# Kernel optimization log

Hardware: AMD Instinct MI355X
Metric: run time of the kernel (lower is better)

The kernel has to match this reference:

```python
import jax, jax.numpy as jnp
import numpy as np

B, D, H, W = 2, 256, 64, 64
NH = 4
EPS = 1e-5


def _ln(x, g, b):
    # LayerNorm over channel dim of NCHW tensor (matches permute->LN(C)->permute)
    mu = jnp.mean(x, axis=1, keepdims=True)
    var = jnp.mean((x - mu) ** 2, axis=1, keepdims=True)
    xn = (x - mu) * jax.lax.rsqrt(var + EPS)
    return xn * g[None, :, None, None] + b[None, :, None, None]


def _conv1x1(x, w, b):
    # w: (out_c, in_c)
    return jnp.einsum('bchw,oc->bohw', x, w) + b[None, :, None, None]


def _dwconv3x3(x, w, b):
    # depthwise 3x3, w: (C, 1, 3, 3)
    y = jax.lax.conv_general_dilated(
        x, w, window_strides=(1, 1), padding='SAME',
        dimension_numbers=('NCHW', 'OIHW', 'NCHW'), feature_group_count=D)
    return y + b[None, :, None, None]


def setup_inputs() -> dict:
    key = jax.random.key(0)
    ks = jax.random.split(key, 12)
    sc = 0.02

    def n(k, shape):
        return jax.random.normal(k, shape, dtype=jnp.float32) * sc

    return {
        'image_embedding': jax.random.normal(ks[0], (B, D, H, W), dtype=jnp.float32),
        'guide': jax.random.normal(ks[1], (B, D, H, W), dtype=jnp.float32),
        'ln1_g': jnp.ones((D,), jnp.float32), 'ln1_b': jnp.zeros((D,), jnp.float32),
        'ln2_g': jnp.ones((D,), jnp.float32), 'ln2_b': jnp.zeros((D,), jnp.float32),
        'qw1': n(ks[2], (D, D)), 'qb1': jnp.zeros((D,), jnp.float32),
        'qw2': n(ks[3], (D, 1, 3, 3)), 'qb2': jnp.zeros((D,), jnp.float32),
        'kw1': n(ks[4], (D, D)), 'kb1': jnp.zeros((D,), jnp.float32),
        'kw2': n(ks[5], (D, 1, 3, 3)), 'kb2': jnp.zeros((D,), jnp.float32),
        'vw1': n(ks[6], (D, D)), 'vb1': jnp.zeros((D,), jnp.float32),
        'vw2': n(ks[7], (D, 1, 3, 3)), 'vb2': jnp.zeros((D,), jnp.float32),
        'ow': n(ks[8], (D, D)), 'ob': jnp.zeros((D,), jnp.float32),
    }


def reference(image_embedding, guide, ln1_g, ln1_b, ln2_g, ln2_b,
              qw1, qb1, qw2, qb2, kw1, kb1, kw2, kb2,
              vw1, vb1, vw2, vb2, ow, ob):
    residual = image_embedding
    x = _ln(image_embedding, ln1_g, ln1_b)
    g = _ln(guide, ln2_g, ln2_b)

    q = _dwconv3x3(_conv1x1(x, qw1, qb1), qw2, qb2)
    k = _dwconv3x3(_conv1x1(g, kw1, kb1), kw2, kb2)
    v = _dwconv3x3(_conv1x1(g, vw1, vb1), vw2, vb2)

    hd = D // NH
    scale = hd ** -0.5

    def to_heads(t):  # (B,C,H,W) -> (B, NH, HW, hd)
        return t.reshape(B, NH, hd, H * W).transpose(0, 1, 3, 2)

    q = to_heads(q) * scale
    k = to_heads(k)
    v = to_heads(v)

    attn = jax.nn.softmax(jnp.einsum('bhnd,bhmd->bhnm', q, k), axis=-1)
    out = jnp.einsum('bhnm,bhmd->bhnd', attn, v)
    out = out.transpose(0, 1, 3, 2).reshape(B, D, H, W)
    out = _conv1x1(out, ow, ob)
    return residual + out
```

## Files before the change

### kernel.cpp

```cpp
#include <hip/hip_runtime.h>
#include <cstdint>
#include <cstddef>

typedef unsigned short u16;
typedef unsigned int u32;
typedef __attribute__((ext_vector_type(8))) short short8;
typedef __attribute__((ext_vector_type(4))) float f32x4;

#define CD 256
#define HWD 4096
#define NHD 4
#define HDD 64

static __device__ __forceinline__ u16 f2b(float f) {
    u32 u = __builtin_bit_cast(u32, f);
    return (u16)((u + 0x7fffu + ((u >> 16) & 1u)) >> 16);
}
static __device__ __forceinline__ float b2f(u16 h) {
    return __builtin_bit_cast(float, (u32)h << 16);
}
static __device__ __forceinline__ u32 pk2(float a, float b) {
    return (u32)f2b(a) | ((u32)f2b(b) << 16);
}
static __device__ __forceinline__ u32 pk2r(float a, float b) {
    u32 ua = __builtin_bit_cast(u32, a) + 0x8000u;
    u32 ub = __builtin_bit_cast(u32, b) + 0x8000u;
    return (ua >> 16) | (ub & 0xffff0000u);
}
static __device__ __forceinline__ float fexp2(float x) {
#if __has_builtin(__builtin_amdgcn_exp2f)
    return __builtin_amdgcn_exp2f(x);
#else
    return __expf(x * 0.69314718056f);
#endif
}
static __device__ __forceinline__ void async16(const void* g, void* l) {
    __builtin_amdgcn_global_load_lds(
        (const __attribute__((address_space(1))) unsigned int*)g,
        (__attribute__((address_space(3))) unsigned int*)l,
        16, 0, 0);
}

__global__ __launch_bounds__(256) void ln_transpose(
    const float* __restrict__ x0, const float* __restrict__ x1,
    const float* __restrict__ g0, const float* __restrict__ b0,
    const float* __restrict__ g1, const float* __restrict__ b1,
    u16* __restrict__ out0, u16* __restrict__ out1)
{
    int bid = blockIdx.x;
    int t = bid >> 7, b = (bid >> 6) & 1, p0 = (bid & 63) << 6;
    const float* x = t ? x1 : x0;
    const float* g = t ? g1 : g0;
    const float* bb = t ? b1 : b0;
    u16* out = t ? out1 : out0;

    int tid = threadIdx.x;
    int tx = tid & 63, ty = tid >> 6;
    const float* xb = x + (size_t)b * CD * HWD + p0 + tx;

    __shared__ float red[2][4][64];
    __shared__ u16 T[256][65];

    float s = 0.f, sq = 0.f;
    #pragma unroll 8
    for (int i = 0; i < 64; ++i) {
        float v = xb[(size_t)(ty * 64 + i) * HWD];
        s += v; sq += v * v;
    }
    red[0][ty][tx] = s; red[1][ty][tx] = sq;
    __syncthreads();
    float st  = red[0][0][tx] + red[0][1][tx] + red[0][2][tx] + red[0][3][tx];
    float sqt = red[1][0][tx] + red[1][1][tx] + red[1][2][tx] + red[1][3][tx];
    float mean = st * (1.f / 256.f);
    float var = sqt * (1.f / 256.f) - mean * mean;
    float rstd = rsqrtf(var + 1e-5f);

    #pragma unroll 8
    for (int i = 0; i < 64; ++i) {
        int c = ty * 64 + i;
        float v = (xb[(size_t)c * HWD] - mean) * rstd * g[c] + bb[c];
        T[c][tx] = f2b(v);
    }
    __syncthreads();

    int pr = tid >> 5, c0 = (tid & 31) * 8;
    #pragma unroll
    for (int pass = 0; pass < 8; ++pass) {
        int p = pass * 8 + pr;
        u16 tmp[8];
        #pragma unroll
        for (int j = 0; j < 8; ++j) tmp[j] = T[c0 + j][p];
        *(uint4*)&out[((size_t)b * HWD + p0 + p) * CD + c0] = *(const uint4*)tmp;
    }
}

__global__ __launch_bounds__(256) void qkv_gemm(
    const u16* __restrict__ xT, const u16* __restrict__ gT,
    const float* __restrict__ qw1, const float* __restrict__ qb1,
    const float* __restrict__ kw1, const float* __restrict__ kb1,
    const float* __restrict__ vw1, const float* __restrict__ vb1,
    u16* __restrict__ q1, u16* __restrict__ k1, u16* __restrict__ v1)
{
    int z = blockIdx.z;
    int mm = z >> 1, b = z & 1;
    const u16* X    = (mm == 0) ? xT : gT;
    const float* W  = (mm == 0) ? qw1 : (mm == 1) ? kw1 : vw1;
    const float* Bi = (mm == 0) ? qb1 : (mm == 1) ? kb1 : vb1;
    u16* Y          = (mm == 0) ? q1 : (mm == 1) ? k1 : v1;

    int n0 = blockIdx.x * 128;
    int p0 = blockIdx.y * 128;

    __shared__ u16 As[128][40];
    __shared__ u16 Bs[128][40];

    int tid = threadIdx.x;
    int lane = tid & 63, w = tid >> 6;
    int wm = w >> 1, wn = w & 1;
    int l15 = lane & 15, quad = lane >> 4;

    f32x4 acc[4][4];
    #pragma unroll
    for (int mi = 0; mi < 4; ++mi)
        #pragma unroll
        for (int nj = 0; nj < 4; ++nj)
            acc[mi][nj] = (f32x4){0.f, 0.f, 0.f, 0.f};

    const u16* Xb = X + (size_t)b * HWD * CD;

    int arow = tid >> 1, akh = (tid & 1) * 16;
    const u16* agp = Xb + (size_t)(p0 + arow) * CD + akh;
    const float* wgp = W + (size_t)(n0 + arow) * CD + akh;

    uint4 ra0 = *(const uint4*)(agp);
    uint4 ra1 = *(const uint4*)(agp + 8);
    float4 rw0 = ((const float4*)wgp)[0], rw1 = ((const float4*)wgp)[1];
    float4 rw2 = ((const float4*)wgp)[2], rw3 = ((const float4*)wgp)[3];

    for (int kt = 0; kt < 8; ++kt) {
        __syncthreads();
        *(uint4*)&As[arow][akh] = ra0;
        *(uint4*)&As[arow][akh + 8] = ra1;
        {
            uint4 qa, qb;
            qa.x = pk2(rw0.x, rw0.y); qa.y = pk2(rw0.z, rw0.w);
            qa.z = pk2(rw1.x, rw1.y); qa.w = pk2(rw1.z, rw1.w);
            qb.x = pk2(rw2.x, rw2.y); qb.y = pk2(rw2.z, rw2.w);
            qb.z = pk2(rw3.x, rw3.y); qb.w = pk2(rw3.z, rw3.w);
            *(uint4*)&Bs[arow][akh] = qa;
            *(uint4*)&Bs[arow][akh + 8] = qb;
        }
        if (kt < 7) {
            const u16* ag2 = agp + (kt + 1) * 32;
            const float* wg2 = wgp + (kt + 1) * 32;
            ra0 = *(const uint4*)(ag2);
            ra1 = *(const uint4*)(ag2 + 8);
            rw0 = ((const float4*)wg2)[0]; rw1 = ((const float4*)wg2)[1];
            rw2 = ((const float4*)wg2)[2]; rw3 = ((const float4*)wg2)[3];
        }
        __syncthreads();

        short8 af[4], bf[4];
        #pragma unroll
        for (int mi = 0; mi < 4; ++mi)
            af[mi] = *(const short8*)&As[wm * 64 + mi * 16 + l15][quad * 8];
        #pragma unroll
        for (int nj = 0; nj < 4; ++nj)
            bf[nj] = *(const short8*)&Bs[wn * 64 + nj * 16 + l15][quad * 8];
        #pragma unroll
        for (int mi = 0; mi < 4; ++mi)
            #pragma unroll
            for (int nj = 0; nj < 4; ++nj)
                acc[mi][nj] = __builtin_amdgcn_mfma_f32_16x16x32_bf16(
                    af[mi], bf[nj], acc[mi][nj], 0, 0, 0);
    }

    u16* Yb = Y + (size_t)b * HWD * CD;
    float bias[4];
    #pragma unroll
    for (int nj = 0; nj < 4; ++nj)
        bias[nj] = Bi[n0 + wn * 64 + nj * 16 + l15];
    #pragma unroll
    for (int mi = 0; mi < 4; ++mi) {
        #pragma unroll
        for (int r = 0; r < 4; ++r) {
            int p = p0 + wm * 64 + mi * 16 + quad * 4 + r;
            #pragma unroll
            for (int nj = 0; nj < 4; ++nj) {
                int ch = n0 + wn * 64 + nj * 16 + l15;
                Yb[(size_t)p * CD + ch] = f2b(acc[mi][nj][r] + bias[nj]);
            }
        }
    }
}

__global__ __launch_bounds__(256) void dwconv_nc(
    const u16* __restrict__ q1, const u16* __restrict__ k1, const u16* __restrict__ v1,
    const float* __restrict__ qw2, const float* __restrict__ qb2,
    const float* __restrict__ kw2, const float* __restrict__ kb2,
    const float* __restrict__ vw2, const float* __restrict__ vb2,
    u16* __restrict__ Q, u16* __restrict__ K, u16* __restrict__ Vt)
{
    int bid = blockIdx.x;
    int which = bid >> 9;
    int b = (bid >> 8) & 1;
    int p0 = (bid & 255) * 16;

    const u16* in = ((which == 0) ? q1 : (which == 1) ? k1 : v1) + (size_t)b * HWD * CD;
    const float* wsrc = (which == 0) ? qw2 : (which == 1) ? kw2 : vw2;
    const float* bsrc = (which == 0) ? qb2 : (which == 1) ? kb2 : vb2;
    float oscale = (which == 0) ? 0.18033688011112042f : 1.0f;

    int c = threadIdx.x;
    float w9[9];
    #pragma unroll
    for (int j = 0; j < 9; ++j) w9[j] = wsrc[c * 9 + j];
    float bias = bsrc[c];

    int h = p0 >> 6, w0 = p0 & 63;

    float accv[16];
    #pragma unroll
    for (int pi = 0; pi < 16; ++pi) accv[pi] = bias;

    #pragma unroll
    for (int dh = -1; dh <= 1; ++dh) {
        int hh = h + dh;
        if (hh < 0 || hh >= 64) continue;
        #pragma unroll
        for (int dw = -1; dw <= 1; ++dw) {
            float wt = w9[(dh + 1) * 3 + (dw + 1)];
            #pragma unroll
            for (int pi = 0; pi < 16; ++pi) {
                int wc = w0 + pi + dw;
                if (wc < 0 || wc >= 64) continue;
                int np = hh * 64 + wc;
                accv[pi] += wt * b2f(in[(size_t)np * CD + c]);
            }
        }
    }

    if (which == 2) {
        u32 w8[8];
        #pragma unroll
        for (int j = 0; j < 8; ++j) w8[j] = pk2(accv[2 * j], accv[2 * j + 1]);
        uint4* dst = (uint4*)(Vt + ((size_t)(b * CD + c)) * HWD + p0);
        dst[0] = make_uint4(w8[0], w8[1], w8[2], w8[3]);
        dst[1] = make_uint4(w8[4], w8[5], w8[6], w8[7]);
    } else {
        u16* out = ((which == 0) ? Q : K) + (size_t)b * HWD * CD;
        #pragma unroll
        for (int pi = 0; pi < 16; ++pi)
            out[(size_t)(p0 + pi) * CD + c] = f2b(accv[pi] * oscale);
    }
}

__global__ __launch_bounds__(256, 2) void attn_kernel(
    const u16* __restrict__ Q, const u16* __restrict__ K,
    const u16* __restrict__ Vt, float* __restrict__ Opart,
    float* __restrict__ Psum)
{
    int qt = blockIdx.x;
    int bh = blockIdx.y;
    int ks = blockIdx.z;
    int b = bh >> 2, nh = bh & 3;

    __shared__ u16 Ks[2][64 * 64];
    __shared__ u16 Vs[2][64 * 64];
    __shared__ u16 Ps[128 * 64];

    int tid = threadIdx.x;
    int lane = tid & 63, w = tid >> 6;
    int l15 = lane & 15, quad = lane >> 4;
    int sw = l15 & 7;

    const u16* Qb = Q + ((size_t)b * HWD) * CD + nh * 64;
    const u16* Kb = K + ((size_t)b * HWD) * CD + nh * 64;
    const u16* Vb = Vt + ((size_t)bh * HDD) * HWD;

    short8 qf[2][2];
    #pragma unroll
    for (int qi = 0; qi < 2; ++qi) {
        const u16* qrow = Qb + (size_t)(qt * 128 + w * 32 + qi * 16 + l15) * CD + quad * 8;
        qf[qi][0] = *(const short8*)(qrow);
        qf[qi][1] = *(const short8*)(qrow + 32);
    }

    int rr = lane >> 3;
    int gseg = (lane & 7) ^ rr;
    const u16* kgb = Kb + (size_t)(ks * 2048 + w * 16 + rr) * CD + gseg * 8;
    const u16* vgb = Vb + (size_t)(w * 16 + rr) * HWD + ks * 2048 + gseg * 8;

    f32x4 acc_o[2][4];
    float psum[2] = {0.f, 0.f};
    #pragma unroll
    for (int qi = 0; qi < 2; ++qi)
        #pragma unroll
        for (int dj = 0; dj < 4; ++dj)
            acc_o[qi][dj] = (f32x4){0.f, 0.f, 0.f, 0.f};

    #pragma unroll
    for (int j = 0; j < 2; ++j) {
        async16(kgb + (size_t)(j * 8) * CD, &Ks[0][(w * 16 + j * 8) * 64]);
        async16(vgb + (size_t)(j * 8) * HWD, &Vs[0][(w * 16 + j * 8) * 64]);
    }

    for (int it = 0; it < 32; ++it) {
        int cur = it & 1;
        __syncthreads();
        if (it + 1 < 32) {
            int nxt = cur ^ 1;
            #pragma unroll
            for (int j = 0; j < 2; ++j) {
                async16(kgb + (size_t)((it + 1) * 64 + j * 8) * CD,
                        &Ks[nxt][(w * 16 + j * 8) * 64]);
                async16(vgb + (size_t)(j * 8) * HWD + (it + 1) * 64,
                        &Vs[nxt][(w * 16 + j * 8) * 64]);
            }
        }

        short8 kf[4][2], vf[4][2];
        #pragma unroll
        for (int nj = 0; nj < 4; ++nj)
            #pragma unroll
            for (int kk = 0; kk < 2; ++kk)
                kf[nj][kk] = *(const short8*)&Ks[cur][(nj * 16 + l15) * 64 +
                                                     (((kk * 4 + quad) ^ sw) << 3)];
        #pragma unroll
        for (int dj = 0; dj < 4; ++dj)
            #pragma unroll
            for (int kk = 0; kk < 2; ++kk)
                vf[dj][kk] = *(const short8*)&Vs[cur][(dj * 16 + l15) * 64 +
                                                     (((kk * 4 + quad) ^ sw) << 3)];

        f32x4 st[4][2];
        #pragma unroll
        for (int nj = 0; nj < 4; ++nj)
            #pragma unroll
            for (int qi = 0; qi < 2; ++qi)
                st[nj][qi] = (f32x4){0.f, 0.f, 0.f, 0.f};
        #pragma unroll
        for (int kk = 0; kk < 2; ++kk)
            #pragma unroll
            for (int nj = 0; nj < 4; ++nj)
                #pragma unroll
                for (int qi = 0; qi < 2; ++qi)
                    st[nj][qi] = __builtin_amdgcn_mfma_f32_16x16x32_bf16(
                        kf[nj][kk], qf[qi][kk], st[nj][qi], 0, 0, 0);

        #pragma unroll
        for (int qi = 0; qi < 2; ++qi) {
            int prow = (w * 32 + qi * 16 + l15) * 64;
            #pragma unroll
            for (int nj = 0; nj < 4; ++nj) {
                float e0 = fexp2(st[nj][qi][0]);
                float e1 = fexp2(st[nj][qi][1]);
                float e2 = fexp2(st[nj][qi][2]);
                float e3 = fexp2(st[nj][qi][3]);
                psum[qi] += (e0 + e1) + (e2 + e3);
                uint2 pw;
                pw.x = pk2r(e0, e1);
                pw.y = pk2r(e2, e3);
                int pcol = (((nj * 2 + (quad >> 1)) ^ sw) << 3) + (quad & 1) * 4;
                *(uint2*)&Ps[prow + pcol] = pw;
            }
        }

        #pragma unroll
        for (int kk = 0; kk < 2; ++kk)
            #pragma unroll
            for (int qi = 0; qi < 2; ++qi) {
                short8 pf = *(const short8*)&Ps[(w * 32 + qi * 16 + l15) * 64 +
                                                (((kk * 4 + quad) ^ sw) << 3)];
                #pragma unroll
                for (int dj = 0; dj < 4; ++dj)
                    acc_o[qi][dj] = __builtin_amdgcn_mfma_f32_16x16x32_bf16(
                        pf, vf[dj][kk], acc_o[qi][dj], 0, 0, 0);
            }
    }

    float* Ob = Opart + (((size_t)ks * 8 + bh) * HWD) * HDD;
    #pragma unroll
    for (int qi = 0; qi < 2; ++qi)
        #pragma unroll
        for (int dj = 0; dj < 4; ++dj)
            #pragma unroll
            for (int r = 0; r < 4; ++r) {
                int n = qt * 128 + w * 32 + qi * 16 + quad * 4 + r;
                Ob[(size_t)n * HDD + dj * 16 + l15] = acc_o[qi][dj][r];
            }

    float* Pb = Psum + ((size_t)ks * 8 + bh) * HWD + qt * 128 + w * 32;
    #pragma unroll
    for (int qi = 0; qi < 2; ++qi) {
        float s = psum[qi];
        s += __shfl_xor(s, 16);
        s += __shfl_xor(s, 32);
        if (quad == 0) Pb[qi * 16 + l15] = s;
    }
}

__global__ __launch_bounds__(256) void out_gemm(
    const float* __restrict__ W, const float* __restrict__ Bi,
    const float* __restrict__ Opart, const float* __restrict__ Psum,
    const float* __restrict__ residual, float* __restrict__ out)
{
    int b = blockIdx.z;
    int m0 = blockIdx.y * 128;
    int n0 = blockIdx.x * 64;

    __shared__ u16 As[128][40];
    __shared__ u16 Bs[64][40];

    int tid = threadIdx.x;
    int lane = tid & 63, w = tid >> 6;
    int wm = w >> 1, wn = w & 1;
    int l15 = lane & 15, quad = lane >> 4;

    f32x4 acc[4][2];
    #pragma unroll
    for (int mi = 0; mi < 4; ++mi)
        #pragma unroll
        for (int nj = 0; nj < 2; ++nj)
            acc[mi][nj] = (f32x4){0.f, 0.f, 0.f, 0.f};

    int arow = tid >> 1, akh = (tid & 1) * 16;
    const float* wgp = W + (size_t)(m0 + arow) * CD + akh;
    int brow = tid >> 2, bseg = (tid & 3) * 8;
    int pn = n0 + brow;

    float4 rw0 = ((const float4*)wgp)[0], rw1 = ((const float4*)wgp)[1];
    float4 rw2 = ((const float4*)wgp)[2], rw3 = ((const float4*)wgp)[3];

    float4 a0, a1, b0, b1; float rinv;
    {
        int c = bseg;
        int bh = b * 4 + (c >> 6), d0 = c & 63;
        const float* O0 = Opart + (((size_t)bh) * HWD + pn) * HDD + d0;
        const float* O1 = Opart + (((size_t)8 + bh) * HWD + pn) * HDD + d0;
        a0 = ((const float4*)O0)[0]; a1 = ((const float4*)O0)[1];
        b0 = ((const float4*)O1)[0]; b1 = ((const float4*)O1)[1];
        float p = Psum[(size_t)bh * HWD + pn] + Psum[((size_t)8 + bh) * HWD + pn];
        rinv = 1.f / p;
    }

    for (int kt = 0; kt < 8; ++kt) {
        __syncthreads();
        {
            uint4 qa, qb;
            qa.x = pk2(rw0.x, rw0.y); qa.y = pk2(rw0.z, rw0.w);
            qa.z = pk2(rw1.x, rw1.y); qa.w = pk2(rw1.z, rw1.w);
            qb.x = pk2(rw2.x, rw2.y); qb.y = pk2(rw2.z, rw2.w);
            qb.z = pk2(rw3.x, rw3.y); qb.w = pk2(rw3.z, rw3.w);
            *(uint4*)&As[arow][akh] = qa;
            *(uint4*)&As[arow][akh + 8] = qb;
        }
        {
            uint4 bb;
            bb.x = pk2((a0.x + b0.x) * rinv, (a0.y + b0.y) * rinv);
            bb.y = pk2((a0.z + b0.z) * rinv, (a0.w + b0.w) * rinv);
            bb.z = pk2((a1.x + b1.x) * rinv, (a1.y + b1.y) * rinv);
            bb.w = pk2((a1.z + b1.z) * rinv, (a1.w + b1.w) * rinv);
            *(uint4*)&Bs[brow][bseg] = bb;
        }
        if (kt < 7) {
            const float* wg2 = wgp + (kt + 1) * 32;
            rw0 = ((const float4*)wg2)[0]; rw1 = ((const float4*)wg2)[1];
            rw2 = ((const float4*)wg2)[2]; rw3 = ((const float4*)wg2)[3];
            int c = (kt + 1) * 32 + bseg;
            int bh = b * 4 + (c >> 6), d0 = c & 63;
            const float* O0 = Opart + (((size_t)bh) * HWD + pn) * HDD + d0;
            const float* O1 = Opart + (((size_t)8 + bh) * HWD + pn) * HDD + d0;
            a0 = ((const float4*)O0)[0]; a1 = ((const float4*)O0)[1];
            b0 = ((const float4*)O1)[0]; b1 = ((const float4*)O1)[1];
            float p = Psum[(size_t)bh * HWD + pn] + Psum[((size_t)8 + bh) * HWD + pn];
            rinv = 1.f / p;
        }
        __syncthreads();

        short8 af[4], bf[2];
        #pragma unroll
        for (int mi = 0; mi < 4; ++mi)
            af[mi] = *(const short8*)&As[wm * 64 + mi * 16 + l15][quad * 8];
        #pragma unroll
        for (int nj = 0; nj < 2; ++nj)
            bf[nj] = *(const short8*)&Bs[wn * 32 + nj * 16 + l15][quad * 8];
        #pragma unroll
        for (int mi = 0; mi < 4; ++mi)
            #pragma unroll
            for (int nj = 0; nj < 2; ++nj)
                acc[mi][nj] = __builtin_amdgcn_mfma_f32_16x16x32_bf16(
                    af[mi], bf[nj], acc[mi][nj], 0, 0, 0);
    }

    #pragma unroll
    for (int mi = 0; mi < 4; ++mi) {
        int mb = m0 + wm * 64 + mi * 16 + quad * 4;
        #pragma unroll
        for (int r = 0; r < 4; ++r) {
            float bias = Bi[mb + r];
            const float* res = residual + (size_t)(b * CD + mb + r) * HWD;
            float* o = out + (size_t)(b * CD + mb + r) * HWD;
            #pragma unroll
            for (int nj = 0; nj < 2; ++nj) {
                int n = n0 + wn * 32 + nj * 16 + l15;
                o[n] = acc[mi][nj][r] + bias + res[n];
            }
        }
    }
}

extern "C" void kernel_launch(void* const* d_in, const int* in_sizes, int n_in,
                              void* d_out, int out_size, void* d_ws, size_t ws_size,
                              hipStream_t stream) {
    (void)in_sizes; (void)n_in; (void)out_size; (void)ws_size;

    const float* image = (const float*)d_in[0];
    const float* guide = (const float*)d_in[1];
    const float* ln1_g = (const float*)d_in[2];
    const float* ln1_b = (const float*)d_in[3];
    const float* ln2_g = (const float*)d_in[4];
    const float* ln2_b = (const float*)d_in[5];
    const float* qw1 = (const float*)d_in[6];
    const float* qb1 = (const float*)d_in[7];
    const float* qw2 = (const float*)d_in[8];
    const float* qb2 = (const float*)d_in[9];
    const float* kw1 = (const float*)d_in[10];
    const float* kb1 = (const float*)d_in[11];
    const float* kw2 = (const float*)d_in[12];
    const float* kb2 = (const float*)d_in[13];
    const float* vw1 = (const float*)d_in[14];
    const float* vb1 = (const float*)d_in[15];
    const float* vw2 = (const float*)d_in[16];
    const float* vb2 = (const float*)d_in[17];
    const float* ow  = (const float*)d_in[18];
    const float* ob  = (const float*)d_in[19];
    float* out = (float*)d_out;

    char* ws = (char*)d_ws;
    u16* xT    = (u16*)(ws + (size_t)0  * (1 << 20));
    u16* gT    = (u16*)(ws + (size_t)4  * (1 << 20));
    u16* q1    = (u16*)(ws + (size_t)8  * (1 << 20));
    u16* k1    = (u16*)(ws + (size_t)12 * (1 << 20));
    u16* v1    = (u16*)(ws + (size_t)16 * (1 << 20));
    u16* Qh    = (u16*)(ws + (size_t)20 * (1 << 20));
    u16* Kh    = (u16*)(ws + (size_t)24 * (1 << 20));
    u16* Vt    = (u16*)(ws + (size_t)28 * (1 << 20));
    float* Opart = (float*)(ws + (size_t)0  * (1 << 20));
    float* Psum  = (float*)(ws + (size_t)16 * (1 << 20));

    ln_transpose<<<dim3(256), dim3(256), 0, stream>>>(
        image, guide, ln1_g, ln1_b, ln2_g, ln2_b, xT, gT);

    qkv_gemm<<<dim3(2, 32, 6), dim3(256), 0, stream>>>(
        xT, gT, qw1, qb1, kw1, kb1, vw1, vb1, q1, k1, v1);

    dwconv_nc<<<dim3(1536), dim3(256), 0, stream>>>(
        q1, k1, v1, qw2, qb2, kw2, kb2, vw2, vb2, Qh, Kh, Vt);

    attn_kernel<<<dim3(32, 8, 2), dim3(256), 0, stream>>>(Qh, Kh, Vt, Opart, Psum);

    out_gemm<<<dim3(64, 2, 2), dim3(256), 0, stream>>>(
        ow, ob, Opart, Psum, image, out);
}
```

Measured before the change: 195.5 us.

## Enlarge attention query tile, split keys four ways, store partial outputs in bf16

The attention kernel now handles 256 queries per block (64 per wave) and splits the key range into four chunks of 1024 instead of two of 2048. This doubles the reuse of each K/V tile loaded into shared memory and keeps the grid size the same. Partial outputs are written as bf16 instead of fp32, and out_gemm sums four partials to cut the traffic for writing and reading them back. The depthwise conv loads each input row once into registers and reuses it across the three taps. The cost is higher register pressure from the larger accumulator tile, a bigger Ps buffer in shared memory, and some precision lost to bf16 partials.

```diff
diff --git a/kernel.cpp b/kernel.cpp
--- a/kernel.cpp
+++ b/kernel.cpp
@@ -224,20 +224,21 @@
     for (int pi = 0; pi < 16; ++pi) accv[pi] = bias;
 
     #pragma unroll
-    for (int dh = -1; dh <= 1; ++dh) {
-        int hh = h + dh;
+    for (int dh = 0; dh < 3; ++dh) {
+        int hh = h + dh - 1;
         if (hh < 0 || hh >= 64) continue;
-        #pragma unroll
-        for (int dw = -1; dw <= 1; ++dw) {
-            float wt = w9[(dh + 1) * 3 + (dw + 1)];
-            #pragma unroll
-            for (int pi = 0; pi < 16; ++pi) {
-                int wc = w0 + pi + dw;
-                if (wc < 0 || wc >= 64) continue;
-                int np = hh * 64 + wc;
-                accv[pi] += wt * b2f(in[(size_t)np * CD + c]);
-            }
-        }
+        const u16* rp = in + ((size_t)hh * 64) * CD + c;
+        float r[18];
+        r[0] = (w0 > 0) ? b2f(rp[(size_t)(w0 - 1) * CD]) : 0.f;
+        #pragma unroll
+        for (int j = 1; j <= 16; ++j)
+            r[j] = b2f(rp[(size_t)(w0 - 1 + j) * CD]);
+        r[17] = (w0 < 48) ? b2f(rp[(size_t)(w0 + 16) * CD]) : 0.f;
+
+        float wa = w9[dh * 3 + 0], wb = w9[dh * 3 + 1], wc = w9[dh * 3 + 2];
+        #pragma unroll
+        for (int pi = 0; pi < 16; ++pi)
+            accv[pi] += wa * r[pi] + wb * r[pi + 1] + wc * r[pi + 2];
     }
 
     if (which == 2) {
@@ -257,7 +258,7 @@
 
 __global__ __launch_bounds__(256, 2) void attn_kernel(
     const u16* __restrict__ Q, const u16* __restrict__ K,
-    const u16* __restrict__ Vt, float* __restrict__ Opart,
+    const u16* __restrict__ Vt, u16* __restrict__ Opart,
     float* __restrict__ Psum)
 {
     int qt = blockIdx.x;
@@ -265,9 +266,9 @@
     int ks = blockIdx.z;
     int b = bh >> 2, nh = bh & 3;
 
-    __shared__ u16 Ks[2][64 * 64];
-    __shared__ u16 Vs[2][64 * 64];
-    __shared__ u16 Ps[128 * 64];
+    __shared__ u16 Ks_[2][64 * 64];
+    __shared__ u16 Vs_[2][64 * 64];
+    __shared__ u16 Ps[256 * 64];
 
     int tid = threadIdx.x;
     int lane = tid & 63, w = tid >> 6;
@@ -278,85 +279,74 @@
     const u16* Kb = K + ((size_t)b * HWD) * CD + nh * 64;
     const u16* Vb = Vt + ((size_t)bh * HDD) * HWD;
 
-    short8 qf[2][2];
-    #pragma unroll
-    for (int qi = 0; qi < 2; ++qi) {
-        const u16* qrow = Qb + (size_t)(qt * 128 + w * 32 + qi * 16 + l15) * CD + quad * 8;
+    short8 qf[4][2];
+    #pragma unroll
+    for (int qi = 0; qi < 4; ++qi) {
+        const u16* qrow = Qb + (size_t)(qt * 256 + w * 64 + qi * 16 + l15) * CD + quad * 8;
         qf[qi][0] = *(const short8*)(qrow);
         qf[qi][1] = *(const short8*)(qrow + 32);
     }
 
     int rr = lane >> 3;
     int gseg = (lane & 7) ^ rr;
-    const u16* kgb = Kb + (size_t)(ks * 2048 + w * 16 + rr) * CD + gseg * 8;
-    const u16* vgb = Vb + (size_t)(w * 16 + rr) * HWD + ks * 2048 + gseg * 8;
-
-    f32x4 acc_o[2][4];
-    float psum[2] = {0.f, 0.f};
-    #pragma unroll
-    for (int qi = 0; qi < 2; ++qi)
+    const u16* kgb = Kb + (size_t)(ks * 1024 + w * 16 + rr) * CD + gseg * 8;
+    const u16* vgb = Vb + (size_t)(w * 16 + rr) * HWD + ks * 1024 + gseg * 8;
+
+    f32x4 acc_o[4][4];
+    float psum[4] = {0.f, 0.f, 0.f, 0.f};
+    #pragma unroll
+    for (int qi = 0; qi < 4; ++qi)
         #pragma unroll
         for (int dj = 0; dj < 4; ++dj)
             acc_o[qi][dj] = (f32x4){0.f, 0.f, 0.f, 0.f};
 
     #pragma unroll
     for (int j = 0; j < 2; ++j) {
-        async16(kgb + (size_t)(j * 8) * CD, &Ks[0][(w * 16 + j * 8) * 64]);
-        async16(vgb + (size_t)(j * 8) * HWD, &Vs[0][(w * 16 + j * 8) * 64]);
-    }
-
-    for (int it = 0; it < 32; ++it) {
+        async16(kgb + (size_t)(j * 8) * CD, &Ks_[0][(w * 16 + j * 8) * 64]);
+        async16(vgb + (size_t)(j * 8) * HWD, &Vs_[0][(w * 16 + j * 8) * 64]);
+    }
+
+    for (int it = 0; it < 16; ++it) {
         int cur = it & 1;
         __syncthreads();
-        if (it + 1 < 32) {
+        if (it + 1 < 16) {
             int nxt = cur ^ 1;
             #pragma unroll
             for (int j = 0; j < 2; ++j) {
                 async16(kgb + (size_t)((it + 1) * 64 + j * 8) * CD,
-                        &Ks[nxt][(w * 16 + j * 8) * 64]);
+                        &Ks_[nxt][(w * 16 + j * 8) * 64]);
                 async16(vgb + (size_t)(j * 8) * HWD + (it + 1) * 64,
-                        &Vs[nxt][(w * 16 + j * 8) * 64]);
-            }
-        }
-
-        short8 kf[4][2], vf[4][2];
+                        &Vs_[nxt][(w * 16 + j * 8) * 64]);
+            }
+        }
+
+        short8 kf[4][2];
         #pragma unroll
         for (int nj = 0; nj < 4; ++nj)
             #pragma unroll
             for (int kk = 0; kk < 2; ++kk)
-                kf[nj][kk] = *(const short8*)&Ks[cur][(nj * 16 + l15) * 64 +
-                                                     (((kk * 4 + quad) ^ sw) << 3)];
-        #pragma unroll
-        for (int dj = 0; dj < 4; ++dj)
+                kf[nj][kk] = *(const short8*)&Ks_[cur][(nj * 16 + l15) * 64 +
+                                                      (((kk * 4 + quad) ^ sw) << 3)];
+
+        #pragma unroll
+        for (int qi = 0; qi < 4; ++qi) {
+            f32x4 st[4];
+            #pragma unroll
+            for (int nj = 0; nj < 4; ++nj) st[nj] = (f32x4){0.f, 0.f, 0.f, 0.f};
             #pragma unroll
             for (int kk = 0; kk < 2; ++kk)
-                vf[dj][kk] = *(const short8*)&Vs[cur][(dj * 16 + l15) * 64 +
-                                                     (((kk * 4 + quad) ^ sw) << 3)];
-
-        f32x4 st[4][2];
-        #pragma unroll
-        for (int nj = 0; nj < 4; ++nj)
-            #pragma unroll
-            for (int qi = 0; qi < 2; ++qi)
-                st[nj][qi] = (f32x4){0.f, 0.f, 0.f, 0.f};
-        #pragma unroll
-        for (int kk = 0; kk < 2; ++kk)
-            #pragma unroll
-            for (int nj = 0; nj < 4; ++nj)
                 #pragma unroll
-                for (int qi = 0; qi < 2; ++qi)
-                    st[nj][qi] = __builtin_amdgcn_mfma_f32_16x16x32_bf16(
-                        kf[nj][kk], qf[qi][kk], st[nj][qi], 0, 0, 0);
-
-        #pragma unroll
-        for (int qi = 0; qi < 2; ++qi) {
-            int prow = (w * 32 + qi * 16 + l15) * 64;
+                for (int nj = 0; nj < 4; ++nj)
+                    st[nj] = __builtin_amdgcn_mfma_f32_16x16x32_bf16(
+                        kf[nj][kk], qf[qi][kk], st[nj], 0, 0, 0);
+
+            int prow = (w * 64 + qi * 16 + l15) * 64;
             #pragma unroll
             for (int nj = 0; nj < 4; ++nj) {
-                float e0 = fexp2(st[nj][qi][0]);
-                float e1 = fexp2(st[nj][qi][1]);
-                float e2 = fexp2(st[nj][qi][2]);
-                float e3 = fexp2(st[nj][qi][3]);
+                float e0 = fexp2(st[nj][0]);
+                float e1 = fexp2(st[nj][1]);
+                float e2 = fexp2(st[nj][2]);
+                float e3 = fexp2(st[nj][3]);
                 psum[qi] += (e0 + e1) + (e2 + e3);
                 uint2 pw;
                 pw.x = pk2r(e0, e1);
@@ -366,11 +356,19 @@
             }
         }
 
+        short8 vf[4][2];
+        #pragma unroll
+        for (int dj = 0; dj < 4; ++dj)
+            #pragma unroll
+            for (int kk = 0; kk < 2; ++kk)
+                vf[dj][kk] = *(const short8*)&Vs_[cur][(dj * 16 + l15) * 64 +
+                                                      (((kk * 4 + quad) ^ sw) << 3)];
+
         #pragma unroll
         for (int kk = 0; kk < 2; ++kk)
             #pragma unroll
-            for (int qi = 0; qi < 2; ++qi) {
-                short8 pf = *(const short8*)&Ps[(w * 32 + qi * 16 + l15) * 64 +
+            for (int qi = 0; qi < 4; ++qi) {
+                short8 pf = *(const short8*)&Ps[(w * 64 + qi * 16 + l15) * 64 +
                                                 (((kk * 4 + quad) ^ sw) << 3)];
                 #pragma unroll
                 for (int dj = 0; dj < 4; ++dj)
@@ -379,20 +377,20 @@
             }
     }
 
-    float* Ob = Opart + (((size_t)ks * 8 + bh) * HWD) * HDD;
-    #pragma unroll
-    for (int qi = 0; qi < 2; ++qi)
+    u16* Ob = Opart + (((size_t)ks * 8 + bh) * HWD) * HDD;
+    #pragma unroll
+    for (int qi = 0; qi < 4; ++qi)
         #pragma unroll
         for (int dj = 0; dj < 4; ++dj)
             #pragma unroll
             for (int r = 0; r < 4; ++r) {
-                int n = qt * 128 + w * 32 + qi * 16 + quad * 4 + r;
-                Ob[(size_t)n * HDD + dj * 16 + l15] = acc_o[qi][dj][r];
-            }
-
-    float* Pb = Psum + ((size_t)ks * 8 + bh) * HWD + qt * 128 + w * 32;
-    #pragma unroll
-    for (int qi = 0; qi < 2; ++qi) {
+                int n = qt * 256 + w * 64 + qi * 16 + quad * 4 + r;
+                Ob[(size_t)n * HDD + dj * 16 + l15] = f2b(acc_o[qi][dj][r]);
+            }
+
+    float* Pb = Psum + ((size_t)ks * 8 + bh) * HWD + qt * 256 + w * 64;
+    #pragma unroll
+    for (int qi = 0; qi < 4; ++qi) {
         float s = psum[qi];
         s += __shfl_xor(s, 16);
         s += __shfl_xor(s, 32);
@@ -402,7 +400,7 @@
 
 __global__ __launch_bounds__(256) void out_gemm(
     const float* __restrict__ W, const float* __restrict__ Bi,
-    const float* __restrict__ Opart, const float* __restrict__ Psum,
+    const u16* __restrict__ Opart, const float* __restrict__ Psum,
     const float* __restrict__ residual, float* __restrict__ out)
 {
     int b = blockIdx.z;
@@ -432,15 +430,16 @@
     float4 rw0 = ((const float4*)wgp)[0], rw1 = ((const float4*)wgp)[1];
     float4 rw2 = ((const float4*)wgp)[2], rw3 = ((const float4*)wgp)[3];
 
-    float4 a0, a1, b0, b1; float rinv;
+    uint4 ro[4]; float rinv;
     {
         int c = bseg;
         int bh = b * 4 + (c >> 6), d0 = c & 63;
-        const float* O0 = Opart + (((size_t)bh) * HWD + pn) * HDD + d0;
-        const float* O1 = Opart + (((size_t)8 + bh) * HWD + pn) * HDD + d0;
-        a0 = ((const float4*)O0)[0]; a1 = ((const float4*)O0)[1];
-        b0 = ((const float4*)O1)[0]; b1 = ((const float4*)O1)[1];
-        float p = Psum[(size_t)bh * HWD + pn] + Psum[((size_t)8 + bh) * HWD + pn];
+        float p = 0.f;
+        #pragma unroll
+        for (int s = 0; s < 4; ++s) {
+            ro[s] = *(const uint4*)&Opart[(((size_t)s * 8 + bh) * HWD + pn) * HDD + d0];
+            p += Psum[((size_t)s * 8 + bh) * HWD + pn];
+        }
         rinv = 1.f / p;
     }
 
@@ -456,11 +455,21 @@
             *(uint4*)&As[arow][akh + 8] = qb;
         }
         {
+            float v[8];
+            #pragma unroll
+            for (int j = 0; j < 8; ++j) v[j] = 0.f;
+            #pragma unroll
+            for (int s = 0; s < 4; ++s) {
+                u16 t[8];
+                *(uint4*)t = ro[s];
+                #pragma unroll
+                for (int j = 0; j < 8; ++j) v[j] += b2f(t[j]);
+            }
             uint4 bb;
-            bb.x = pk2((a0.x + b0.x) * rinv, (a0.y + b0.y) * rinv);
-            bb.y = pk2((a0.z + b0.z) * rinv, (a0.w + b0.w) * rinv);
-            bb.z = pk2((a1.x + b1.x) * rinv, (a1.y + b1.y) * rinv);
-            bb.w = pk2((a1.z + b1.z) * rinv, (a1.w + b1.w) * rinv);
+            bb.x = pk2(v[0] * rinv, v[1] * rinv);
+            bb.y = pk2(v[2] * rinv, v[3] * rinv);
+            bb.z = pk2(v[4] * rinv, v[5] * rinv);
+            bb.w = pk2(v[6] * rinv, v[7] * rinv);
             *(uint4*)&Bs[brow][bseg] = bb;
         }
         if (kt < 7) {
@@ -469,11 +478,12 @@
             rw2 = ((const float4*)wg2)[2]; rw3 = ((const float4*)wg2)[3];
             int c = (kt + 1) * 32 + bseg;
             int bh = b * 4 + (c >> 6), d0 = c & 63;
-            const float* O0 = Opart + (((size_t)bh) * HWD + pn) * HDD + d0;
-            const float* O1 = Opart + (((size_t)8 + bh) * HWD + pn) * HDD + d0;
-            a0 = ((const float4*)O0)[0]; a1 = ((const float4*)O0)[1];
-            b0 = ((const float4*)O1)[0]; b1 = ((const float4*)O1)[1];
-            float p = Psum[(size_t)bh * HWD + pn] + Psum[((size_t)8 + bh) * HWD + pn];
+            float p = 0.f;
+            #pragma unroll
+            for (int s = 0; s < 4; ++s) {
+                ro[s] = *(const uint4*)&Opart[(((size_t)s * 8 + bh) * HWD + pn) * HDD + d0];
+                p += Psum[((size_t)s * 8 + bh) * HWD + pn];
+            }
             rinv = 1.f / p;
         }
         __syncthreads();
@@ -546,8 +556,8 @@
     u16* Qh    = (u16*)(ws + (size_t)20 * (1 << 20));
     u16* Kh    = (u16*)(ws + (size_t)24 * (1 << 20));
     u16* Vt    = (u16*)(ws + (size_t)28 * (1 << 20));
-    float* Opart = (float*)(ws + (size_t)0  * (1 << 20));
-    float* Psum  = (float*)(ws + (size_t)16 * (1 << 20));
+    u16*   Opart = (u16*)(ws + (size_t)0  * (1 << 20));
+    float* Psum  = (float*)(ws + (size_t)18 * (1 << 20));
 
     ln_transpose<<<dim3(256), dim3(256), 0, stream>>>(
         image, guide, ln1_g, ln1_b, ln2_g, ln2_b, xT, gT);
@@ -558,7 +568,7 @@
     dwconv_nc<<<dim3(1536), dim3(256), 0, stream>>>(
         q1, k1, v1, qw2, qb2, kw2, kb2, vw2, vb2, Qh, Kh, Vt);
 
-    attn_kernel<<<dim3(32, 8, 2), dim3(256), 0, stream>>>(Qh, Kh, Vt, Opart, Psum);
+    attn_kernel<<<dim3(16, 8, 4), dim3(256), 0, stream>>>(Qh, Kh, Vt, Opart, Psum);
 
     out_gemm<<<dim3(64, 2, 2), dim3(256), 0, stream>>>(
         ow, ob, Opart, Psum, image, out);
```

After: 188.9 us. 1.03x faster.
